# Kernel tuning notes

Measured on AMD Instinct MI355X. Metric: run time of the kernel, lower is better.

The kernel has to match this reference:

```python
import math
import jax, jax.numpy as jnp
import numpy as np

H = 12
D_MODEL = 768
D_K = D_MODEL // H
B, S = 2, 2048


def setup_inputs() -> dict:
    key = jax.random.key(0)
    ks = jax.random.split(key, 12)
    sc = 0.02
    inp = {
        "query": jax.random.normal(ks[0], (B, S, D_MODEL), jnp.float32),
        "key": jax.random.normal(ks[1], (B, S, D_MODEL), jnp.float32),
        "value": jax.random.normal(ks[2], (B, S, D_MODEL), jnp.float32),
        # causal mask [B, S, S]: 1 where attendable
        "mask": jnp.broadcast_to(jnp.tril(jnp.ones((S, S), jnp.int32)), (B, S, S)),
        "Wq": sc * jax.random.normal(ks[3], (D_MODEL, D_MODEL), jnp.float32),
        "bq": jnp.zeros((D_MODEL,), jnp.float32),
        "Wk": sc * jax.random.normal(ks[4], (D_MODEL, D_MODEL), jnp.float32),
        "bk": jnp.zeros((D_MODEL,), jnp.float32),
        "Wv": sc * jax.random.normal(ks[5], (D_MODEL, D_MODEL), jnp.float32),
        "bv": jnp.zeros((D_MODEL,), jnp.float32),
        "Wo": sc * jax.random.normal(ks[6], (D_MODEL, D_MODEL), jnp.float32),
        "bo": jnp.zeros((D_MODEL,), jnp.float32),
    }
    return inp


def reference(query, key, value, mask, Wq, bq, Wk, bk, Wv, bv, Wo, bo):
    b, s, _ = query.shape
    # linear projections (torch Linear: x @ W.T + b), split into heads
    def proj(x, W, bias):
        return (x @ W.T + bias).reshape(b, s, H, D_K).transpose(0, 2, 1, 3)  # [B,H,S,Dk]

    q = proj(query, Wq, bq)
    k = proj(key, Wk, bk)
    v = proj(value, Wv, bv)

    scores = jnp.einsum("bhqd,bhkd->bhqk", q, k) / math.sqrt(D_K)  # [B,H,S,S]
    # exponential time-decay bias over key positions 1..S, shape [1,1,1,S]
    time = jnp.exp(-jnp.arange(1, s + 1, dtype=scores.dtype))[None, None, None, :]
    scores = jnp.where(mask[:, None, :, :] == 0, jnp.asarray(-1e9, scores.dtype), scores)
    p_attn = jax.nn.softmax(scores - time, axis=-1)
    x = jnp.einsum("bhqk,bhkd->bhqd", p_attn, v)  # [B,H,S,Dk]
    x = x.transpose(0, 2, 1, 3).reshape(b, s, H * D_K)
    return x @ Wo.T + bo
```

## Files before the change

### kernel.cpp

```cpp
#include <hip/hip_runtime.h>
#include <hip/hip_bf16.h>
#include <math.h>

typedef __bf16 bf16;
typedef __attribute__((ext_vector_type(8))) __bf16 bf16x8;
typedef __attribute__((ext_vector_type(4))) __bf16 bf16x4;
typedef __attribute__((ext_vector_type(4))) float floatx4;

#define NH 12
#define DK 64
#define DM 768
#define NB 2
#define SEQ 2048
#define MTOT (NB * SEQ)
#define WELEM (DM * DM)
#define XELEM (MTOT * DM)

#define QSCALE 0.1803368801111832f
#define LOG2E 1.4426950408889634f

static __device__ __forceinline__ bf16x8 load8(const bf16* p) {
    return *(const bf16x8*)p;
}
static __device__ __forceinline__ float4 ld4(const float* p) {
    return *(const float4*)p;
}
static __device__ __forceinline__ bf16x8 cvt8(const float4 a, const float4 b) {
    bf16x8 r;
    r[0] = (bf16)a.x; r[1] = (bf16)a.y; r[2] = (bf16)a.z; r[3] = (bf16)a.w;
    r[4] = (bf16)b.x; r[5] = (bf16)b.y; r[6] = (bf16)b.z; r[7] = (bf16)b.w;
    return r;
}
static __device__ __forceinline__ float fast_exp2(float x) {
#if __has_builtin(__builtin_amdgcn_exp2f)
    return __builtin_amdgcn_exp2f(x);
#else
    return __expf(x * 0.6931471805599453f);
#endif
}
static __device__ __forceinline__ void async16(const bf16* g, bf16* l) {
    __builtin_amdgcn_global_load_lds((const __attribute__((address_space(1))) void*)g,
                                     (__attribute__((address_space(3))) void*)l,
                                     16, 0, 0);
}

__global__ __launch_bounds__(256) void cvt_kernel(
    const float* __restrict__ wq, const float* __restrict__ wk,
    const float* __restrict__ wv, const float* __restrict__ wo,
    const float* __restrict__ xq, const float* __restrict__ xk, const float* __restrict__ xv,
    bf16* __restrict__ Wb, bf16* __restrict__ Wob,
    bf16* __restrict__ Xqb, bf16* __restrict__ Xkb, bf16* __restrict__ Xvb) {
    const int g = blockIdx.x * 256 + threadIdx.x;
    const int PW = WELEM / 8;
    const int PX = XELEM / 8;
    if (g < 4 * PW) {
        const int wi = g / PW;
        const int rem = g - wi * PW;
        const int n = rem / 96;
        const int t = rem - n * 96;
        const int s = t >> 3;
        const int j = t & 7;
        const float* src = (wi == 0) ? wq : (wi == 1) ? wk : (wi == 2) ? wv : wo;
        bf16* dst = (wi < 3) ? (Wb + (size_t)wi * WELEM) : Wob;
        const float* p = src + (size_t)n * DM + s * 64 + j * 8;
        *(bf16x8*)(dst + (size_t)n * DM + s * 64 + ((j ^ (n & 7)) * 8)) = cvt8(ld4(p), ld4(p + 4));
    } else {
        const int gx = g - 4 * PW;
        const int xi = gx / PX;
        const int rem = gx - xi * PX;
        const int m = rem / 96;
        const int t = rem - m * 96;
        const int s = t >> 3;
        const int j = t & 7;
        const float* src = (xi == 0) ? xq : (xi == 1) ? xk : xv;
        bf16* dst = (xi == 0) ? Xqb : (xi == 1) ? Xkb : Xvb;
        const float* p = src + (size_t)m * DM + s * 64 + j * 8;
        *(bf16x8*)(dst + (size_t)m * DM + s * 64 + ((j ^ (m & 7)) * 8)) = cvt8(ld4(p), ld4(p + 4));
    }
}

__global__ __launch_bounds__(256, 3) void qkv_kernel(
    const bf16* __restrict__ Xqb, const bf16* __restrict__ Xkb, const bf16* __restrict__ Xvb,
    const bf16* __restrict__ Wb,
    const float* __restrict__ bq, const float* __restrict__ bk, const float* __restrict__ bv,
    bf16* __restrict__ Oq, bf16* __restrict__ Ok, bf16* __restrict__ Ov) {
    __shared__ __align__(16) bf16 SM[2 * 64 * 64 + 2 * 128 * 64];
    bf16* As0 = SM;
    bf16* Bs0 = SM + 8192;

    const int tid = threadIdx.x;
    const int id = blockIdx.x;
    const int xcd = id & 7;
    const int sl = id >> 3;
    const int z = sl / 48;
    const int r = sl % 48;
    const int m0 = (xcd * 8 + r / 6) * 64;
    const int n0 = (r % 6) * 128;

    const bf16* X = (z == 0) ? Xqb : (z == 1) ? Xkb : Xvb;
    const bf16* W = Wb + (size_t)z * WELEM;
    const float* bias = (z == 0) ? bq : (z == 1) ? bk : bv;
    bf16* out = (z == 0) ? Oq : (z == 1) ? Ok : Ov;

    const int wv = tid >> 6;
    const int wm = wv >> 1, wn = wv & 1;
    const int lane = tid & 63;
    const int ln = lane & 15;
    const int kq = lane >> 4;
    const int drow = lane >> 3;
    const int dcol = (lane & 7) * 8;

    floatx4 acc[2][4];
#pragma unroll
    for (int i = 0; i < 2; i++)
#pragma unroll
        for (int j = 0; j < 4; j++) acc[i][j] = (floatx4){0.f, 0.f, 0.f, 0.f};

#pragma unroll
    for (int it = 0; it < 2; it++)
        async16(X + (size_t)(m0 + wv * 16 + it * 8 + drow) * DM + dcol,
                As0 + (wv * 16 + it * 8) * 64);
#pragma unroll
    for (int it = 0; it < 4; it++)
        async16(W + (size_t)(n0 + wv * 32 + it * 8 + drow) * DM + dcol,
                Bs0 + (wv * 32 + it * 8) * 64);

    for (int k = 0; k < 12; k++) {
        __syncthreads();
        const bf16* Ap = As0 + (k & 1) * 4096;
        const bf16* Bp = Bs0 + (k & 1) * 8192;
        if (k < 11) {
            const int kc = (k + 1) * 64;
            bf16* An = As0 + ((k + 1) & 1) * 4096;
            bf16* Bn = Bs0 + ((k + 1) & 1) * 8192;
#pragma unroll
            for (int it = 0; it < 2; it++)
                async16(X + (size_t)(m0 + wv * 16 + it * 8 + drow) * DM + kc + dcol,
                        An + (wv * 16 + it * 8) * 64);
#pragma unroll
            for (int it = 0; it < 4; it++)
                async16(W + (size_t)(n0 + wv * 32 + it * 8 + drow) * DM + kc + dcol,
                        Bn + (wv * 32 + it * 8) * 64);
        }
#pragma unroll
        for (int ks = 0; ks < 2; ks++) {
            const int jb = (ks * 4 + kq) ^ (ln & 7);
            bf16x8 af[2], bfm[4];
#pragma unroll
            for (int mt = 0; mt < 2; mt++)
                af[mt] = *(const bf16x8*)&Ap[(wm * 32 + mt * 16 + ln) * 64 + jb * 8];
#pragma unroll
            for (int nt = 0; nt < 4; nt++)
                bfm[nt] = *(const bf16x8*)&Bp[(wn * 64 + nt * 16 + ln) * 64 + jb * 8];
#pragma unroll
            for (int mt = 0; mt < 2; mt++)
#pragma unroll
                for (int nt = 0; nt < 4; nt++)
                    acc[mt][nt] = __builtin_amdgcn_mfma_f32_16x16x32_bf16(af[mt], bfm[nt], acc[mt][nt], 0, 0, 0);
        }
    }

    float bv4[4];
#pragma unroll
    for (int nt = 0; nt < 4; nt++) bv4[nt] = bias[n0 + wn * 64 + nt * 16 + ln];

    if (z < 2) {
        const float qs = (z == 0) ? QSCALE : 1.0f;
        __syncthreads();
        bf16 (*E)[136] = (bf16(*)[136])SM;
#pragma unroll
        for (int mt = 0; mt < 2; mt++)
#pragma unroll
            for (int nt = 0; nt < 4; nt++)
#pragma unroll
                for (int r2 = 0; r2 < 4; r2++)
                    E[wm * 32 + mt * 16 + kq * 4 + r2][wn * 64 + nt * 16 + ln] =
                        (bf16)((acc[mt][nt][r2] + bv4[nt]) * qs);
        __syncthreads();
        const int row = tid >> 2;
        const int cb = (tid & 3) * 32;
        const int m = m0 + row;
        const int b = m >> 11;
        const int s = m & (SEQ - 1);
        const int h = (n0 + cb) >> 6;
        const int d = (n0 + cb) & 63;
        bf16* op = &out[((size_t)(b * NH + h) * SEQ + s) * DK + d];
#pragma unroll
        for (int q2 = 0; q2 < 4; q2++)
            *(bf16x8*)(op + q2 * 8) = *(bf16x8*)&E[row][cb + q2 * 8];
    } else {
        __syncthreads();
        bf16 (*E)[72] = (bf16(*)[72])SM;
#pragma unroll
        for (int nt = 0; nt < 4; nt++)
#pragma unroll
            for (int mt = 0; mt < 2; mt++) {
                bf16x4 v;
#pragma unroll
                for (int r2 = 0; r2 < 4; r2++) v[r2] = (bf16)(acc[mt][nt][r2] + bv4[nt]);
                *(bf16x4*)&E[wn * 64 + nt * 16 + ln][wm * 32 + mt * 16 + kq * 4] = v;
            }
        __syncthreads();
        const int row = tid >> 1;
        const int sc = (tid & 1) * 32;
        const int b = m0 >> 11;
        const int s0 = m0 & (SEQ - 1);
        const int h = (n0 >> 6) + (row >> 6);
        const int d = row & 63;
        bf16* op = &out[(size_t)(b * NH + h) * DK * SEQ + (size_t)d * SEQ + s0 + sc];
#pragma unroll
        for (int q2 = 0; q2 < 4; q2++)
            *(bf16x8*)(op + q2 * 8) = *(bf16x8*)&E[row][sc + q2 * 8];
    }
}


#define QK_BODY(FIRSTC)                                                        \
    _Pragma("unroll")                                                          \
    for (int ks = 0; ks < 8; ks++) {                                           \
        const bf16x8 a0 = *(bf16x8*)&Ks[ks * 16 + ln][kq * 8];                 \
        const bf16x8 a1 = *(bf16x8*)&Ks[ks * 16 + ln][32 + kq * 8];            \
        floatx4 t = (floatx4){0.f, 0.f, 0.f, 0.f};                             \
        t = __builtin_amdgcn_mfma_f32_16x16x32_bf16(a0, qa0, t, 0, 0, 0);      \
        t = __builtin_amdgcn_mfma_f32_16x16x32_bf16(a1, qa1, t, 0, 0, 0);      \
        const int kbase = k0 + (ks >> 1) * 32 + (ks & 1) * 4 + kq * 8;         \
        _Pragma("unroll")                                                      \
        for (int r = 0; r < 4; r++) {                                          \
            const int kg = kbase + r;                                          \
            float sv = t[r];                                                   \
            if (FIRSTC) sv -= __expf(-(float)(kg + 1)) * LOG2E;                \
            float pf = fast_exp2(sv);                                          \
            if (lastc && kg > qgl) pf = 0.f;                                   \
            lsum += pf;                                                        \
            pa[ks >> 1][(ks & 1) * 4 + r] = (bf16)pf;                          \
        }                                                                      \
    }

__global__ __launch_bounds__(256) void attn_kernel(const bf16* __restrict__ Q,
                                                   const bf16* __restrict__ K,
                                                   const bf16* __restrict__ Vt,
                                                   bf16* __restrict__ Xout) {
    __shared__ bf16 Ks[128][72];
    __shared__ bf16 Vs[64][136];

    const int tid = threadIdx.x;
    const int wv = tid >> 6;
    const int lane = tid & 63;
    const int ln = lane & 15;
    const int kq = lane >> 4;
    const int krow = tid >> 1;
    const int kprow = (krow & 0x60) | ((krow & 4) << 2) | ((krow & 24) >> 1) | (krow & 3);
    const int kcol = (tid & 1) * 32;
    const int vrow = tid >> 2;
    const int vcol = (tid & 3) * 32;

    const int bidx = blockIdx.x;
    const int rk = (bidx < 256 || bidx >= 512) ? bidx : 767 - bidx;
    const int x = 31 - (rk / 24);
    const int bh = rk % 24;

    const int q0 = x * 64;
    const int qbase = q0 + wv * 16;
    const int nch = (x >> 1) + 1;

    const bf16* Qb = Q + (size_t)bh * SEQ * DK;
    const bf16* Kb = K + (size_t)bh * SEQ * DK;
    const bf16* Vb = Vt + (size_t)bh * SEQ * DK;

    const bf16x8 qa0 = load8(&Qb[(size_t)(qbase + ln) * DK + kq * 8]);
    const bf16x8 qa1 = load8(&Qb[(size_t)(qbase + ln) * DK + 32 + kq * 8]);

    bf16x8 kx[4], vx[4];
#pragma unroll
    for (int q = 0; q < 4; q++) {
        kx[q] = load8(&Kb[(size_t)krow * DK + kcol + q * 8]);
        vx[q] = load8(&Vb[(size_t)vrow * SEQ + vcol + q * 8]);
    }

    float lsum = 0.f;
    floatx4 Oacc[4];
#pragma unroll
    for (int nt = 0; nt < 4; nt++) Oacc[nt] = (floatx4){0.f, 0.f, 0.f, 0.f};

    const int qgl = qbase + ln;

    for (int c = 0; c < nch; c++) {
        const int k0 = c * 128;
        __syncthreads();
#pragma unroll
        for (int q = 0; q < 4; q++) {
            *(bf16x8*)&Ks[kprow][kcol + q * 8] = kx[q];
            *(bf16x8*)&Vs[vrow][vcol + q * 8] = vx[q];
        }
        __syncthreads();
        if (c + 1 < nch) {
            const int kn = k0 + 128;
#pragma unroll
            for (int q = 0; q < 4; q++) {
                kx[q] = load8(&Kb[(size_t)(kn + krow) * DK + kcol + q * 8]);
                vx[q] = load8(&Vb[(size_t)vrow * SEQ + kn + vcol + q * 8]);
            }
        }

        const bool lastc = (c == nch - 1);
        bf16x8 pa[4];
        if (c == 0) {
            QK_BODY(true)
        } else {
            QK_BODY(false)
        }

        __builtin_amdgcn_s_setprio(1);
#pragma unroll
        for (int nt = 0; nt < 4; nt++) {
#pragma unroll
            for (int seg = 0; seg < 4; seg++) {
                const bf16x8 vb = *(bf16x8*)&Vs[nt * 16 + ln][seg * 32 + kq * 8];
                Oacc[nt] = __builtin_amdgcn_mfma_f32_16x16x32_bf16(pa[seg], vb, Oacc[nt], 0, 0, 0);
            }
        }
        __builtin_amdgcn_s_setprio(0);
    }

    lsum += __shfl_xor(lsum, 16, 64);
    lsum += __shfl_xor(lsum, 32, 64);
    float rl[4];
#pragma unroll
    for (int r = 0; r < 4; r++) rl[r] = 1.f / __shfl(lsum, kq * 4 + r, 64);

    __syncthreads();
    bf16 (*E)[72] = (bf16(*)[72])Ks;
    const int erow = tid >> 2;
    const int ecb = (tid & 3) * 16;
#pragma unroll
    for (int nt = 0; nt < 4; nt++) {
#pragma unroll
        for (int r = 0; r < 4; r++)
            E[wv * 16 + kq * 4 + r][nt * 16 + ln] = (bf16)(Oacc[nt][r] * rl[r]);
    }
    __syncthreads();
    const int b = bh / NH;
    const int h = bh - b * NH;
    const int q = q0 + erow;
    const int j0 = (tid & 3) * 2;
    const int key = erow & 7;
    bf16* rowp = &Xout[((size_t)(b * SEQ + q)) * DM + h * DK];
    *(bf16x8*)(rowp + ((j0 ^ key) * 8)) = *(bf16x8*)&E[erow][ecb];
    *(bf16x8*)(rowp + (((j0 + 1) ^ key) * 8)) = *(bf16x8*)&E[erow][ecb + 8];
}

__global__ __launch_bounds__(256, 3) void outproj_kernel(const bf16* __restrict__ X,
                                                         const bf16* __restrict__ W,
                                                         const float* __restrict__ bias,
                                                         float* __restrict__ out) {
    __shared__ __align__(16) bf16 SM[2 * 64 * 64 + 2 * 128 * 64];
    bf16* As0 = SM;
    bf16* Bs0 = SM + 8192;

    const int tid = threadIdx.x;
    const int id = blockIdx.x;
    const int xcd = id & 7;
    const int sl = id >> 3;
    const int m0 = (xcd * 8 + sl / 6) * 64;
    const int n0 = (sl % 6) * 128;

    const int wv = tid >> 6;
    const int wm = wv >> 1, wn = wv & 1;
    const int lane = tid & 63;
    const int ln = lane & 15;
    const int kq = lane >> 4;
    const int drow = lane >> 3;
    const int dcol = (lane & 7) * 8;

    floatx4 acc[2][4];
#pragma unroll
    for (int i = 0; i < 2; i++)
#pragma unroll
        for (int j = 0; j < 4; j++) acc[i][j] = (floatx4){0.f, 0.f, 0.f, 0.f};

#pragma unroll
    for (int it = 0; it < 2; it++)
        async16(X + (size_t)(m0 + wv * 16 + it * 8 + drow) * DM + dcol,
                As0 + (wv * 16 + it * 8) * 64);
#pragma unroll
    for (int it = 0; it < 4; it++)
        async16(W + (size_t)(n0 + wv * 32 + it * 8 + drow) * DM + dcol,
                Bs0 + (wv * 32 + it * 8) * 64);

    for (int k = 0; k < 12; k++) {
        __syncthreads();
        const bf16* Ap = As0 + (k & 1) * 4096;
        const bf16* Bp = Bs0 + (k & 1) * 8192;
        if (k < 11) {
            const int kc = (k + 1) * 64;
            bf16* An = As0 + ((k + 1) & 1) * 4096;
            bf16* Bn = Bs0 + ((k + 1) & 1) * 8192;
#pragma unroll
            for (int it = 0; it < 2; it++)
                async16(X + (size_t)(m0 + wv * 16 + it * 8 + drow) * DM + kc + dcol,
                        An + (wv * 16 + it * 8) * 64);
#pragma unroll
            for (int it = 0; it < 4; it++)
                async16(W + (size_t)(n0 + wv * 32 + it * 8 + drow) * DM + kc + dcol,
                        Bn + (wv * 32 + it * 8) * 64);
        }
#pragma unroll
        for (int ks = 0; ks < 2; ks++) {
            const int jb = (ks * 4 + kq) ^ (ln & 7);
            bf16x8 af[2], bfm[4];
#pragma unroll
            for (int mt = 0; mt < 2; mt++)
                af[mt] = *(const bf16x8*)&Ap[(wm * 32 + mt * 16 + ln) * 64 + jb * 8];
#pragma unroll
            for (int nt = 0; nt < 4; nt++)
                bfm[nt] = *(const bf16x8*)&Bp[(wn * 64 + nt * 16 + ln) * 64 + jb * 8];
#pragma unroll
            for (int mt = 0; mt < 2; mt++)
#pragma unroll
                for (int nt = 0; nt < 4; nt++)
                    acc[mt][nt] = __builtin_amdgcn_mfma_f32_16x16x32_bf16(af[mt], bfm[nt], acc[mt][nt], 0, 0, 0);
        }
    }

#pragma unroll
    for (int nt = 0; nt < 4; nt++) {
        const int n = n0 + wn * 64 + nt * 16 + ln;
        const float bval = bias[n];
#pragma unroll
        for (int mt = 0; mt < 2; mt++)
#pragma unroll
            for (int r2 = 0; r2 < 4; r2++) {
                const int m = m0 + wm * 32 + mt * 16 + kq * 4 + r2;
                out[(size_t)m * DM + n] = acc[mt][nt][r2] + bval;
            }
    }
}

extern "C" void kernel_launch(void* const* d_in, const int* in_sizes, int n_in,
                              void* d_out, int out_size, void* d_ws, size_t ws_size,
                              hipStream_t stream) {
    const float* query = (const float*)d_in[0];
    const float* key   = (const float*)d_in[1];
    const float* value = (const float*)d_in[2];
    const float* Wq = (const float*)d_in[4];
    const float* bq = (const float*)d_in[5];
    const float* Wk = (const float*)d_in[6];
    const float* bk = (const float*)d_in[7];
    const float* Wv = (const float*)d_in[8];
    const float* bv = (const float*)d_in[9];
    const float* Wo = (const float*)d_in[10];
    const float* bo = (const float*)d_in[11];
    float* out = (float*)d_out;

    bf16* Qws  = (bf16*)d_ws;
    bf16* Kws  = Qws + XELEM;
    bf16* Vtws = Kws + XELEM;
    bf16* Xws  = Vtws + XELEM;
    bf16* Wob  = Xws + XELEM;
    bf16* Xvb  = Wob + WELEM;

    bf16* Wb  = (bf16*)out;
    bf16* Xkb = (bf16*)out + 3 * WELEM;

    bf16* Xqb = Xws;

    const int ncvt = (4 * (WELEM / 8) + 3 * (XELEM / 8)) / 256;
    cvt_kernel<<<ncvt, 256, 0, stream>>>(Wq, Wk, Wv, Wo, query, key, value,
                                         Wb, Wob, Xqb, Xkb, Xvb);

    qkv_kernel<<<1152, 256, 0, stream>>>(Xqb, Xkb, Xvb, Wb, bq, bk, bv,
                                         Qws, Kws, Vtws);

    attn_kernel<<<768, 256, 0, stream>>>(Qws, Kws, Vtws, Xws);

    outproj_kernel<<<384, 256, 0, stream>>>(Xws, Wob, bo, out);
}
```

Before: 187.4 us.

## Load K fragments directly from global memory and double-buffer V in LDS

The attention kernel stops staging K tiles in shared memory. Each lane now loads its QK^T MFMA operands straight from global memory, using a permuted row index that reproduces the old swizzled LDS layout. V is double-buffered in LDS, so each chunk needs one barrier instead of two, and the V store and prefetch come after the QK/softmax phase. This cuts LDS traffic and synchronisation, but each wave issues many uncoalesced, latency-bound global K loads inside the compute loop with no prefetch, relying on L2/cache hits because the 4 waves share the same K rows.

Result: slower. 224.4 us (+19.8%).

```diff
diff --git a/kernel.cpp b/kernel.cpp
--- a/kernel.cpp
+++ b/kernel.cpp
@@ -218,8 +218,8 @@
 #define QK_BODY(FIRSTC)                                                        \
     _Pragma("unroll")                                                          \
     for (int ks = 0; ks < 8; ks++) {                                           \
-        const bf16x8 a0 = *(bf16x8*)&Ks[ks * 16 + ln][kq * 8];                 \
-        const bf16x8 a1 = *(bf16x8*)&Ks[ks * 16 + ln][32 + kq * 8];            \
+        const bf16x8 a0 = load8(Kp + (size_t)(k0 + (ks >> 1) * 32 + (ks & 1) * 4) * DK); \
+        const bf16x8 a1 = load8(Kp + (size_t)(k0 + (ks >> 1) * 32 + (ks & 1) * 4) * DK + 32); \
         floatx4 t = (floatx4){0.f, 0.f, 0.f, 0.f};                             \
         t = __builtin_amdgcn_mfma_f32_16x16x32_bf16(a0, qa0, t, 0, 0, 0);      \
         t = __builtin_amdgcn_mfma_f32_16x16x32_bf16(a1, qa1, t, 0, 0, 0);      \
@@ -240,17 +240,13 @@
                                                    const bf16* __restrict__ K,
                                                    const bf16* __restrict__ Vt,
                                                    bf16* __restrict__ Xout) {
-    __shared__ bf16 Ks[128][72];
-    __shared__ bf16 Vs[64][136];
+    __shared__ bf16 Vs[2][64][136];
 
     const int tid = threadIdx.x;
     const int wv = tid >> 6;
     const int lane = tid & 63;
     const int ln = lane & 15;
     const int kq = lane >> 4;
-    const int krow = tid >> 1;
-    const int kprow = (krow & 0x60) | ((krow & 4) << 2) | ((krow & 24) >> 1) | (krow & 3);
-    const int kcol = (tid & 1) * 32;
     const int vrow = tid >> 2;
     const int vcol = (tid & 3) * 32;
 
@@ -270,12 +266,12 @@
     const bf16x8 qa0 = load8(&Qb[(size_t)(qbase + ln) * DK + kq * 8]);
     const bf16x8 qa1 = load8(&Qb[(size_t)(qbase + ln) * DK + 32 + kq * 8]);
 
-    bf16x8 kx[4], vx[4];
-#pragma unroll
-    for (int q = 0; q < 4; q++) {
-        kx[q] = load8(&Kb[(size_t)krow * DK + kcol + q * 8]);
-        vx[q] = load8(&Vb[(size_t)vrow * SEQ + vcol + q * 8]);
-    }
+    const int pln = ((ln >> 2) << 3) | (ln & 3);
+    const bf16* Kp = Kb + (size_t)pln * DK + kq * 8;
+
+    bf16x8 vx[4];
+#pragma unroll
+    for (int q = 0; q < 4; q++) vx[q] = load8(&Vb[(size_t)vrow * SEQ + vcol + q * 8]);
 
     float lsum = 0.f;
     floatx4 Oacc[4];
@@ -286,23 +282,8 @@
 
     for (int c = 0; c < nch; c++) {
         const int k0 = c * 128;
-        __syncthreads();
-#pragma unroll
-        for (int q = 0; q < 4; q++) {
-            *(bf16x8*)&Ks[kprow][kcol + q * 8] = kx[q];
-            *(bf16x8*)&Vs[vrow][vcol + q * 8] = vx[q];
-        }
-        __syncthreads();
-        if (c + 1 < nch) {
-            const int kn = k0 + 128;
-#pragma unroll
-            for (int q = 0; q < 4; q++) {
-                kx[q] = load8(&Kb[(size_t)(kn + krow) * DK + kcol + q * 8]);
-                vx[q] = load8(&Vb[(size_t)vrow * SEQ + kn + vcol + q * 8]);
-            }
-        }
-
         const bool lastc = (c == nch - 1);
+
         bf16x8 pa[4];
         if (c == 0) {
             QK_BODY(true)
@@ -310,12 +291,24 @@
             QK_BODY(false)
         }
 
+#pragma unroll
+        for (int q = 0; q < 4; q++) *(bf16x8*)&Vs[c & 1][vrow][vcol + q * 8] = vx[q];
+
+        if (c + 1 < nch) {
+            const int kn = k0 + 128;
+#pragma unroll
+            for (int q = 0; q < 4; q++)
+                vx[q] = load8(&Vb[(size_t)vrow * SEQ + kn + vcol + q * 8]);
+        }
+
+        __syncthreads();
+
         __builtin_amdgcn_s_setprio(1);
 #pragma unroll
         for (int nt = 0; nt < 4; nt++) {
 #pragma unroll
             for (int seg = 0; seg < 4; seg++) {
-                const bf16x8 vb = *(bf16x8*)&Vs[nt * 16 + ln][seg * 32 + kq * 8];
+                const bf16x8 vb = *(bf16x8*)&Vs[c & 1][nt * 16 + ln][seg * 32 + kq * 8];
                 Oacc[nt] = __builtin_amdgcn_mfma_f32_16x16x32_bf16(pa[seg], vb, Oacc[nt], 0, 0, 0);
             }
         }
@@ -329,7 +322,7 @@
     for (int r = 0; r < 4; r++) rl[r] = 1.f / __shfl(lsum, kq * 4 + r, 64);
 
     __syncthreads();
-    bf16 (*E)[72] = (bf16(*)[72])Ks;
+    bf16 (*E)[72] = (bf16(*)[72])Vs;
     const int erow = tid >> 2;
     const int ecb = (tid & 3) * 16;
 #pragma unroll
```
